# Optimization experiments

Measured on AMD Instinct MI355X. Metric: run time of the kernel, lower is better.

The kernel has to match this reference:

```python
import jax, jax.numpy as jnp
import numpy as np

N_NODES = 50000
N_EDGES = 500000
IN_CH = 128
OUT_CH = 64
HEADS = 4


def setup_inputs() -> dict:
    key = jax.random.key(0)
    ks = jax.random.split(key, 9)
    x = jax.random.normal(ks[0], (N_NODES, IN_CH), dtype=jnp.float32)
    edge_index = jax.random.randint(ks[1], (2, N_EDGES), 0, N_NODES, dtype=jnp.int64)
    edge_weights = jax.random.uniform(ks[2], (N_EDGES, 1), dtype=jnp.float32)
    # xavier-uniform params, stored as [in, out] so y = x @ W
    def xavier(k, shape):
        fan_in, fan_out = shape
        lim = float(np.sqrt(6.0 / (fan_in + fan_out)))
        return jax.random.uniform(k, shape, minval=-lim, maxval=lim, dtype=jnp.float32)
    Wq = xavier(ks[3], (IN_CH, OUT_CH * HEADS))
    Wk = xavier(ks[4], (IN_CH, OUT_CH * HEADS))
    Wv = xavier(ks[5], (IN_CH, OUT_CH * HEADS))
    We = xavier(ks[6], (1, HEADS))
    Wout = xavier(ks[7], (OUT_CH * HEADS, OUT_CH))
    b_out = jnp.zeros((OUT_CH,), dtype=jnp.float32)
    return {"x": x, "edge_index": edge_index, "edge_weights": edge_weights,
            "Wq": Wq, "Wk": Wk, "Wv": Wv, "We": We, "Wout": Wout, "b_out": b_out}


def reference(x, edge_index, edge_weights, Wq, Wk, Wv, We, Wout, b_out):
    num_nodes = x.shape[0]
    src = edge_index[0]
    tgt = edge_index[1]
    x_src = x[src]                                    # [E, in]
    x_tgt = x[tgt]                                    # [E, in]
    q = (x_tgt @ Wq).reshape(-1, HEADS, OUT_CH)       # [E, H, C]
    k = (x_src @ Wk).reshape(-1, HEADS, OUT_CH)
    v = (x_src @ Wv).reshape(-1, HEADS, OUT_CH)
    attn = jnp.sum(q * k, axis=-1) / jnp.sqrt(jnp.float32(OUT_CH))  # [E, H]
    attn = attn + edge_weights @ We                   # [E, H]
    attn = jax.nn.leaky_relu(attn, negative_slope=0.2)
    attn = jax.nn.softmax(attn, axis=0)               # global softmax over edges (as in source)
    weighted_v = attn[..., None] * v                  # [E, H, C]
    out = jax.ops.segment_sum(weighted_v, tgt, num_segments=num_nodes)  # [N, H, C]
    out = out.reshape(num_nodes, HEADS * OUT_CH) @ Wout + b_out         # [N, out]
    if x.shape == out.shape:
        out = out + x
    return out
```

## Files before the change

kernel.cpp:

```cpp
#include <hip/hip_runtime.h>
#include <hip/hip_bf16.h>
#include <hip/hip_fp16.h>

#define N_NODES 50000
#define N_EDGES 500000
#define IN_CH   128
#define D       256
#define UDIM    512
#define OUT_CH  64
#define HEADS   4
#define NC      49
#define PCAP    448
#define DEPTH   4

#define NB_X16  6250
#define NB_HIST 1954
#define NB_MB   256
#define NB_ZB   128
#define NB_GEMM 1564
#define NB_SCAT 1954
#define NB_K4   (NB_GEMM + NB_SCAT)
#define NB_OUT  782

typedef _Float16 half8 __attribute__((ext_vector_type(8)));
typedef _Float16 half2_t __attribute__((ext_vector_type(2)));
typedef float   floatx4 __attribute__((ext_vector_type(4)));

typedef __attribute__((address_space(1))) const void as1_void;
typedef __attribute__((address_space(3))) void as3_void;

__device__ __forceinline__ void gll16(const void* g, void* l) {
    __builtin_amdgcn_global_load_lds((as1_void*)g, (as3_void*)l, 16, 0, 0);
}

__device__ __forceinline__ float dpp_xor1(float x) {
    return __int_as_float(__builtin_amdgcn_mov_dpp(__float_as_int(x), 0xB1, 0xf, 0xf, true));
}
__device__ __forceinline__ float dpp_xor2(float x) {
    return __int_as_float(__builtin_amdgcn_mov_dpp(__float_as_int(x), 0x4E, 0xf, 0xf, true));
}

__global__ __launch_bounds__(256) void k1_prep_kernel(const float* __restrict__ x,
                                                      __half* __restrict__ x16,
                                                      const int* __restrict__ ei,
                                                      int* __restrict__ cnt,
                                                      double* __restrict__ S,
                                                      const float* __restrict__ Wq,
                                                      const float* __restrict__ Wk,
                                                      const float* __restrict__ Wv,
                                                      const float* __restrict__ Wout,
                                                      __half* __restrict__ M16t,
                                                      __half* __restrict__ Zc16t) {
    __shared__ float sbuf[4][64];
    const int b = blockIdx.x, tid = threadIdx.x;
    if (b < NB_X16) {
        int i = b * 256 + tid;
        if (i < HEADS) S[i] = 0.0;
        int k = i * 4;
        if (k < N_NODES * IN_CH) {
            float4 v = *(const float4*)(x + k);
            union { __half2 h[2]; uint2 u; } pk;
            pk.h[0] = __floats2half2_rn(v.x, v.y);
            pk.h[1] = __floats2half2_rn(v.z, v.w);
            *(uint2*)(x16 + k) = pk.u;
        }
    } else if (b < NB_X16 + NB_HIST) {
        int e = (b - NB_X16) * 256 + tid;
        if (e < N_EDGES) atomicAdd(&cnt[ei[N_EDGES + e]], 1);
    } else if (b < NB_X16 + NB_HIST + NB_MB) {
        const int r = (b - NB_X16 - NB_HIST) * 2 + (tid >> 7);
        const int i = tid & 127;
        const int h = r >> 7, j = r & 127;
        float* buf = sbuf[tid >> 7];
        if (i < 64) buf[i] = Wk[(size_t)j * D + h * 64 + i];
        __syncthreads();
        const float4* qr = (const float4*)(Wq + (size_t)i * D + h * 64);
        float s = 0.f;
        #pragma unroll
        for (int c4 = 0; c4 < 16; ++c4) {
            float4 q = qr[c4];
            s += q.x * buf[c4 * 4] + q.y * buf[c4 * 4 + 1]
               + q.z * buf[c4 * 4 + 2] + q.w * buf[c4 * 4 + 3];
        }
        M16t[(size_t)r * IN_CH + i] = __float2half(s);
    } else {
        const int r = (b - NB_X16 - NB_HIST - NB_MB) * 4 + (tid >> 6);
        const int c = tid & 63;
        const int h = r >> 7, i = r & 127;
        float* buf = sbuf[tid >> 6];
        buf[c] = Wv[(size_t)i * D + h * 64 + c];
        __syncthreads();
        float s = 0.f;
        #pragma unroll 8
        for (int j = 0; j < 64; ++j)
            s += buf[j] * Wout[(size_t)(h * 64 + j) * OUT_CH + c];
        Zc16t[(size_t)c * UDIM + r] = __float2half(s);
    }
}

__global__ __launch_bounds__(256) void k2_scan_reduce_kernel(const int* __restrict__ cnt,
                                                             int* __restrict__ csum) {
    const int b = blockIdx.x, tid = threadIdx.x;
    const int lane = tid & 63, wid = tid >> 6;
    int s = 0;
    int idx0 = b * 1024 + tid * 4;
    #pragma unroll
    for (int i = 0; i < 4; ++i) {
        int idx = idx0 + i;
        if (idx < N_NODES) s += cnt[idx];
    }
    #pragma unroll
    for (int m = 1; m < 64; m <<= 1) s += __shfl_xor(s, m, 64);
    __shared__ int w4[4];
    if (lane == 0) w4[wid] = s;
    __syncthreads();
    if (tid == 0) csum[b] = w4[0] + w4[1] + w4[2] + w4[3];
}

__global__ __launch_bounds__(256) void k3_scan_chunks_kernel(int* __restrict__ cnt,
                                                             const int* __restrict__ csum,
                                                             int* __restrict__ rp) {
    __shared__ int stop[64];
    __shared__ int wsum[4];
    const int b = blockIdx.x, tid = threadIdx.x;
    const int lane = tid & 63, wid = tid >> 6;
    if (tid < 64) stop[tid] = (tid < NC) ? csum[tid] : 0;
    __syncthreads();
    int base = 0;
    for (int w = 0; w < b; ++w) base += stop[w];
    int v[4];
    const int idx0 = b * 1024 + tid * 4;
    #pragma unroll
    for (int i = 0; i < 4; ++i) {
        int idx = idx0 + i;
        v[i] = (idx < N_NODES) ? cnt[idx] : 0;
    }
    int tsum = v[0] + v[1] + v[2] + v[3];
    int x = tsum;
    #pragma unroll
    for (int d = 1; d < 64; d <<= 1) {
        int y = __shfl_up(x, d, 64);
        if (lane >= d) x += y;
    }
    if (lane == 63) wsum[wid] = x;
    __syncthreads();
    int woff = 0;
    for (int w = 0; w < wid; ++w) woff += wsum[w];
    int excl = base + woff + x - tsum;
    #pragma unroll
    for (int i = 0; i < 4; ++i) {
        int idx = idx0 + i;
        if (idx < N_NODES) { rp[idx] = excl; cnt[idx] = excl; }
        excl += v[i];
    }
}

__global__ __launch_bounds__(256) void k4_gemmu_scatter_kernel(const __half* __restrict__ x16,
                                                               const __half* __restrict__ M16t,
                                                               __half* __restrict__ u16,
                                                               const int* __restrict__ ei,
                                                               const float* __restrict__ ew,
                                                               int* __restrict__ cnt,
                                                               int2* __restrict__ payload) {
    __shared__ __half Bm[128][136];
    const int tid = threadIdx.x;
    const int b = blockIdx.x;
    const int glo = (int)(((long long)b * NB_GEMM) / NB_K4);
    const int ghi = (int)(((long long)(b + 1) * NB_GEMM) / NB_K4);
    if (ghi == glo) {
        int e = (b - glo) * 256 + tid;
        if (e < N_EDGES) {
            int s = ei[e], t = ei[N_EDGES + e];
            int pos = atomicAdd(&cnt[t], 1);
            payload[pos] = make_int2(s, __float_as_int(ew[e]));
        }
        return;
    }
    const int m0 = (glo % 391) * 128;
    const int colbase = (glo / 391) * 128;
    {
        const int r = tid >> 1, part = tid & 1;
        const uint4* sb = (const uint4*)(M16t + (size_t)(colbase + r) * IN_CH + part * 64);
        uint4* db = (uint4*)&Bm[r][part * 64];
        #pragma unroll
        for (int q = 0; q < 8; ++q) db[q] = sb[q];
    }

    const int w = tid >> 6, lane = tid & 63;
    const int mrow = lane & 15, quad = lane >> 4;

    half8 a[2][4];
    #pragma unroll
    for (int mt = 0; mt < 2; ++mt) {
        int row = min(m0 + w * 32 + mt * 16 + mrow, N_NODES - 1);
        const __half* ab = x16 + (size_t)row * IN_CH + quad * 8;
        #pragma unroll
        for (int ks = 0; ks < 4; ++ks) a[mt][ks] = *(const half8*)(ab + ks * 32);
    }
    __syncthreads();

    floatx4 acc[2][8];
    #pragma unroll
    for (int mt = 0; mt < 2; ++mt)
        #pragma unroll
        for (int nt = 0; nt < 8; ++nt)
            acc[mt][nt] = (floatx4){0.f, 0.f, 0.f, 0.f};

    #pragma unroll
    for (int nt = 0; nt < 8; ++nt) {
        #pragma unroll
        for (int ks = 0; ks < 4; ++ks) {
            half8 bfr = *(const half8*)&Bm[nt * 16 + mrow][ks * 32 + quad * 8];
            acc[0][nt] = __builtin_amdgcn_mfma_f32_16x16x32_f16(a[0][ks], bfr, acc[0][nt], 0, 0, 0);
            acc[1][nt] = __builtin_amdgcn_mfma_f32_16x16x32_f16(a[1][ks], bfr, acc[1][nt], 0, 0, 0);
        }
    }
    __syncthreads();
    #pragma unroll
    for (int mt = 0; mt < 2; ++mt)
        #pragma unroll
        for (int nt = 0; nt < 8; ++nt)
            #pragma unroll
            for (int r = 0; r < 4; ++r)
                Bm[w * 32 + mt * 16 + quad * 4 + r][nt * 16 + mrow] = __float2half(acc[mt][nt][r]);
    __syncthreads();
    {
        const int r = tid >> 1, part = tid & 1;
        if (m0 + r < N_NODES) {
            const uint4* s4 = (const uint4*)&Bm[r][part * 64];
            uint4* d4 = (uint4*)(u16 + (size_t)(m0 + r) * UDIM + colbase + part * 64);
            #pragma unroll
            for (int q = 0; q < 8; ++q) d4[q] = s4[q];
        }
    }
}

__global__ __launch_bounds__(256) void edge_fused_kernel(const __half* __restrict__ u16,
                                                         const __half* __restrict__ x16,
                                                         const int* __restrict__ rp,
                                                         const int* __restrict__ cnt,
                                                         const int2* __restrict__ payload,
                                                         const float* __restrict__ We,
                                                         __half* __restrict__ y16,
                                                         double* __restrict__ S) {
    __shared__ __half xring[4][DEPTH][512];
    __shared__ int2 pbuf[PCAP];
    __shared__ float sblk[4];
    const int tid = threadIdx.x;
    const int nodebase = blockIdx.x * 16;

    const int span0 = rp[nodebase];
    const int span1 = cnt[nodebase + 15];
    const int span  = span1 - span0;
    const int span_len = min(span, PCAP);
    for (int i = tid; i < span_len; i += 256) pbuf[i] = payload[span0 + i];
    if (tid < 4) sblk[tid] = 0.f;
    __syncthreads();

    const int w = tid >> 6, lane = tid & 63;
    const int g = lane >> 4;
    const int l16 = lane & 15;
    const int h = l16 >> 2;
    const int q = l16 & 3;
    const int node = nodebase + (tid >> 4);
    const float wev = We[h];

    uint4 ur4[4];
    {
        const uint4* ub = (const uint4*)(u16 + (size_t)node * UDIM + h * 128 + q * 32);
        ur4[0] = ub[0]; ur4[1] = ub[1]; ur4[2] = ub[2]; ur4[3] = ub[3];
    }
    const half2_t* uh = (const half2_t*)ur4;

    half2_t yacc[16];
    #pragma unroll
    for (int t = 0; t < 16; ++t) yacc[t] = (half2_t){(_Float16)0.f, (_Float16)0.f};

    float sacc = 0.f;
    const int start = rp[node];
    const int end = cnt[node];
    const int ng = end - start;

    if (span <= PCAP) {
        int nmax = ng;
        nmax = max(nmax, __shfl_xor(nmax, 16, 64));
        nmax = max(nmax, __shfl_xor(nmax, 32, 64));
        if (nmax > 0) {
            const int chunk_off = (l16 ^ g) * 8;
            auto src_of = [&](int t) -> const __half* {
                int idx = min(start + t, end - 1);
                idx = max(idx, span0);
                int s = pbuf[idx - span0].x;
                return x16 + (size_t)s * IN_CH + chunk_off;
            };
            #pragma unroll
            for (int s = 0; s < DEPTH; ++s)
                gll16(src_of(s), &xring[w][s][0]);

            for (int t = 0; t < nmax; ++t) {
                const int slot = t & (DEPTH - 1);
                asm volatile("s_waitcnt vmcnt(3)" ::: "memory");
                __builtin_amdgcn_sched_barrier(0);
                const uint4* rb = (const uint4*)&xring[w][slot][g * 128 + q * 32];
                uint4 xr0 = rb[0 ^ g];
                uint4 xr1 = rb[1 ^ g];
                uint4 xr2 = rb[2 ^ g];
                uint4 xr3 = rb[3 ^ g];
                asm volatile("s_waitcnt lgkmcnt(0)" ::: "memory");
                __builtin_amdgcn_sched_barrier(0);
                gll16(src_of(t + DEPTH), &xring[w][slot][0]);

                int2 pl;
                {
                    int idx = min(start + t, end - 1);
                    idx = max(idx, span0);
                    pl = pbuf[idx - span0];
                }
                uint4 xr[4] = {xr0, xr1, xr2, xr3};
                const half2_t* xh = (const half2_t*)xr;
                float d0 = 0.f, d1 = 0.f, d2 = 0.f, d3 = 0.f;
                #pragma unroll
                for (int tt = 0; tt < 4; ++tt) {
                    d0 = __builtin_amdgcn_fdot2(uh[tt],      xh[tt],      d0, false);
                    d1 = __builtin_amdgcn_fdot2(uh[tt + 4],  xh[tt + 4],  d1, false);
                    d2 = __builtin_amdgcn_fdot2(uh[tt + 8],  xh[tt + 8],  d2, false);
                    d3 = __builtin_amdgcn_fdot2(uh[tt + 12], xh[tt + 12], d3, false);
                }
                float dot = (d0 + d1) + (d2 + d3);
                dot += dpp_xor1(dot);
                dot += dpp_xor2(dot);
                float l = dot * 0.125f + __int_as_float(pl.y) * wev;
                l = fmaxf(l, 0.2f * l);
                float p = __expf(l);
                if (t < ng) {
                    if (q == 0) sacc += p;
                    half2_t p2 = (half2_t){(_Float16)p, (_Float16)p};
                    #pragma unroll
                    for (int tt = 0; tt < 16; ++tt)
                        yacc[tt] = p2 * xh[tt] + yacc[tt];
                }
            }
        }
    } else {
        auto getpl = [&](int e) -> int2 {
            int idx = e - span0;
            return (idx < PCAP) ? pbuf[idx] : payload[e];
        };
        int2 pl = make_int2(0, 0);
        uint4 xr[4];
        if (start < end) {
            pl = getpl(start);
            const uint4* xb = (const uint4*)(x16 + (size_t)pl.x * IN_CH + q * 32);
            xr[0] = xb[0]; xr[1] = xb[1]; xr[2] = xb[2]; xr[3] = xb[3];
        }
        for (int e = start; e < end; ++e) {
            int2 pln = pl;
            uint4 xrn[4] = {xr[0], xr[1], xr[2], xr[3]};
            if (e + 1 < end) {
                pln = getpl(e + 1);
                const uint4* xb = (const uint4*)(x16 + (size_t)pln.x * IN_CH + q * 32);
                xrn[0] = xb[0]; xrn[1] = xb[1]; xrn[2] = xb[2]; xrn[3] = xb[3];
            }
            const half2_t* xh = (const half2_t*)xr;
            float dot = 0.f;
            #pragma unroll
            for (int t = 0; t < 16; ++t)
                dot = __builtin_amdgcn_fdot2(uh[t], xh[t], dot, false);
            dot += __shfl_xor(dot, 1, 16);
            dot += __shfl_xor(dot, 2, 16);
            float l = dot * 0.125f + __int_as_float(pl.y) * wev;
            l = fmaxf(l, 0.2f * l);
            float p = __expf(l);
            if (q == 0) sacc += p;
            half2_t p2 = (half2_t){(_Float16)p, (_Float16)p};
            #pragma unroll
            for (int t = 0; t < 16; ++t)
                yacc[t] = p2 * xh[t] + yacc[t];
            pl = pln;
            xr[0] = xrn[0]; xr[1] = xrn[1]; xr[2] = xrn[2]; xr[3] = xrn[3];
        }
    }
    {
        uint4* yo = (uint4*)(y16 + (size_t)node * UDIM + h * 128 + q * 32);
        const uint4* ys = (const uint4*)yacc;
        yo[0] = ys[0]; yo[1] = ys[1]; yo[2] = ys[2]; yo[3] = ys[3];
    }
    __syncthreads();
    if (q == 0) atomicAdd(&sblk[h], sacc);
    __syncthreads();
    if (tid < 4) atomicAdd(&S[tid], (double)sblk[tid]);
}

__global__ __launch_bounds__(256) void gemm_out_mfma_kernel(const __half* __restrict__ y16,
                                                            const __half* __restrict__ Zc16t,
                                                            const double* __restrict__ S,
                                                            const float* __restrict__ b_out,
                                                            float* __restrict__ out) {
    const int tid = threadIdx.x;
    const int w = tid >> 6, lane = tid & 63;
    const int mrow = lane & 15, quad = lane >> 4;
    const int row0 = blockIdx.x * 64 + w * 16;

    float invs[4];
    #pragma unroll
    for (int hh = 0; hh < HEADS; ++hh) invs[hh] = (float)(1.0 / S[hh]);

    floatx4 result[4];
    #pragma unroll
    for (int nt = 0; nt < 4; ++nt) result[nt] = (floatx4){0.f, 0.f, 0.f, 0.f};

    for (int h = 0; h < HEADS; ++h) {
        half8 a[4];
        {
            int arow = min(row0 + mrow, N_NODES - 1);
            const __half* ab = y16 + (size_t)arow * UDIM + h * 128 + quad * 8;
            #pragma unroll
            for (int ks = 0; ks < 4; ++ks) a[ks] = *(const half8*)(ab + ks * 32);
        }
        const float inv = invs[h];
        #pragma unroll
        for (int nt = 0; nt < 4; ++nt) {
            floatx4 acc = (floatx4){0.f, 0.f, 0.f, 0.f};
            const __half* bb = Zc16t + (size_t)(nt * 16 + mrow) * UDIM + h * 128 + quad * 8;
            #pragma unroll
            for (int ks = 0; ks < 4; ++ks) {
                half8 bfr = *(const half8*)(bb + ks * 32);
                acc = __builtin_amdgcn_mfma_f32_16x16x32_f16(a[ks], bfr, acc, 0, 0, 0);
            }
            result[nt][0] += inv * acc[0];
            result[nt][1] += inv * acc[1];
            result[nt][2] += inv * acc[2];
            result[nt][3] += inv * acc[3];
        }
    }
    float bcol[4];
    #pragma unroll
    for (int nt = 0; nt < 4; ++nt) bcol[nt] = b_out[nt * 16 + mrow];
    #pragma unroll
    for (int r = 0; r < 4; ++r) {
        int row = row0 + quad * 4 + r;
        if (row < N_NODES) {
            float* dst = out + (size_t)row * OUT_CH;
            #pragma unroll
            for (int nt = 0; nt < 4; ++nt)
                dst[nt * 16 + mrow] = result[nt][r] + bcol[nt];
        }
    }
}

extern "C" void kernel_launch(void* const* d_in, const int* in_sizes, int n_in,
                              void* d_out, int out_size, void* d_ws, size_t ws_size,
                              hipStream_t stream) {
    const float* x     = (const float*)d_in[0];
    const int*   ei    = (const int*)d_in[1];
    const float* ew    = (const float*)d_in[2];
    const float* Wq    = (const float*)d_in[3];
    const float* Wk    = (const float*)d_in[4];
    const float* Wv    = (const float*)d_in[5];
    const float* We    = (const float*)d_in[6];
    const float* Wout  = (const float*)d_in[7];
    const float* b_out = (const float*)d_in[8];
    float* out = (float*)d_out;

    __half* u16   = (__half*)d_ws;
    __half* y16   = u16 + (size_t)N_NODES * UDIM;
    __half* x16   = y16 + (size_t)N_NODES * UDIM;
    double* S     = (double*)(x16 + (size_t)N_NODES * IN_CH);
    __half* M16t  = (__half*)(S + HEADS);
    __half* Zc16t = M16t + UDIM * IN_CH;
    int*    rp    = (int*)(Zc16t + OUT_CH * UDIM);
    int*    cnt   = rp + N_NODES;
    int*    csum  = cnt + N_NODES;
    int2*   payload = (int2*)(csum + 64);

    hipMemsetAsync(cnt, 0, N_NODES * sizeof(int), stream);
    k1_prep_kernel<<<NB_X16 + NB_HIST + NB_MB + NB_ZB, 256, 0, stream>>>(
        x, x16, ei, cnt, S, Wq, Wk, Wv, Wout, M16t, Zc16t);
    k2_scan_reduce_kernel<<<NC, 256, 0, stream>>>(cnt, csum);
    k3_scan_chunks_kernel<<<NC, 256, 0, stream>>>(cnt, csum, rp);
    k4_gemmu_scatter_kernel<<<NB_K4, 256, 0, stream>>>(
        x16, M16t, u16, ei, ew, cnt, payload);
    edge_fused_kernel<<<N_NODES / 16, 256, 0, stream>>>(u16, x16, rp, cnt, payload, We, y16, S);
    gemm_out_mfma_kernel<<<NB_OUT, 256, 0, stream>>>(y16, Zc16t, S, b_out, out);
}
```

Measured before the change: 259.4 us.

## Fuse per-head output projection into edge kernel, add light finalize pass

The edge kernel now keeps its 16-node aggregated rows in LDS and runs the per-head MFMA projection against Zc16t in place, storing per-head partial outputs (N×256 fp16) instead of the full N×512 aggregate. A small finalize kernel then scales each head's partial by the global softmax denominator, sums the heads and adds the bias. This removes the write and re-read of the large y16 buffer and replaces the heavier output GEMM kernel with an elementwise pass. The cost is extra LDS and MFMA work inside the edge kernel, which may lower occupancy, plus fp16 rounding of the per-head partials before normalisation.

New measurement: 237.8 us. 8.3% less time.

```diff
diff --git a/kernel.cpp b/kernel.cpp
--- a/kernel.cpp
+++ b/kernel.cpp
@@ -20,7 +20,6 @@
 #define NB_GEMM 1564
 #define NB_SCAT 1954
 #define NB_K4   (NB_GEMM + NB_SCAT)
-#define NB_OUT  782
 
 typedef _Float16 half8 __attribute__((ext_vector_type(8)));
 typedef _Float16 half2_t __attribute__((ext_vector_type(2)));
@@ -241,9 +240,11 @@
                                                          const int* __restrict__ cnt,
                                                          const int2* __restrict__ payload,
                                                          const float* __restrict__ We,
-                                                         __half* __restrict__ y16,
+                                                         const __half* __restrict__ Zc16t,
+                                                         __half* __restrict__ p16,
                                                          double* __restrict__ S) {
     __shared__ __half xring[4][DEPTH][512];
+    __shared__ __half y_lds[16][520];
     __shared__ int2 pbuf[PCAP];
     __shared__ float sblk[4];
     const int tid = threadIdx.x;
@@ -381,71 +382,54 @@
         }
     }
     {
-        uint4* yo = (uint4*)(y16 + (size_t)node * UDIM + h * 128 + q * 32);
+        uint4* yo = (uint4*)&y_lds[tid >> 4][h * 128 + q * 32];
         const uint4* ys = (const uint4*)yacc;
         yo[0] = ys[0]; yo[1] = ys[1]; yo[2] = ys[2]; yo[3] = ys[3];
     }
-    __syncthreads();
     if (q == 0) atomicAdd(&sblk[h], sacc);
     __syncthreads();
     if (tid < 4) atomicAdd(&S[tid], (double)sblk[tid]);
-}
-
-__global__ __launch_bounds__(256) void gemm_out_mfma_kernel(const __half* __restrict__ y16,
-                                                            const __half* __restrict__ Zc16t,
-                                                            const double* __restrict__ S,
-                                                            const float* __restrict__ b_out,
-                                                            float* __restrict__ out) {
-    const int tid = threadIdx.x;
-    const int w = tid >> 6, lane = tid & 63;
-    const int mrow = lane & 15, quad = lane >> 4;
-    const int row0 = blockIdx.x * 64 + w * 16;
-
-    float invs[4];
-    #pragma unroll
-    for (int hh = 0; hh < HEADS; ++hh) invs[hh] = (float)(1.0 / S[hh]);
-
-    floatx4 result[4];
-    #pragma unroll
-    for (int nt = 0; nt < 4; ++nt) result[nt] = (floatx4){0.f, 0.f, 0.f, 0.f};
-
-    for (int h = 0; h < HEADS; ++h) {
-        half8 a[4];
-        {
-            int arow = min(row0 + mrow, N_NODES - 1);
-            const __half* ab = y16 + (size_t)arow * UDIM + h * 128 + quad * 8;
-            #pragma unroll
-            for (int ks = 0; ks < 4; ++ks) a[ks] = *(const half8*)(ab + ks * 32);
-        }
-        const float inv = invs[h];
+
+    {
+        const int hh = w;
+        const int mrow = lane & 15, quad = lane >> 4;
+        half8 a2[4];
+        #pragma unroll
+        for (int ks = 0; ks < 4; ++ks)
+            a2[ks] = *(const half8*)&y_lds[mrow][hh * 128 + ks * 32 + quad * 8];
         #pragma unroll
         for (int nt = 0; nt < 4; ++nt) {
             floatx4 acc = (floatx4){0.f, 0.f, 0.f, 0.f};
-            const __half* bb = Zc16t + (size_t)(nt * 16 + mrow) * UDIM + h * 128 + quad * 8;
+            const __half* bb = Zc16t + (size_t)(nt * 16 + mrow) * UDIM + hh * 128 + quad * 8;
             #pragma unroll
             for (int ks = 0; ks < 4; ++ks) {
                 half8 bfr = *(const half8*)(bb + ks * 32);
-                acc = __builtin_amdgcn_mfma_f32_16x16x32_f16(a[ks], bfr, acc, 0, 0, 0);
+                acc = __builtin_amdgcn_mfma_f32_16x16x32_f16(a2[ks], bfr, acc, 0, 0, 0);
             }
-            result[nt][0] += inv * acc[0];
-            result[nt][1] += inv * acc[1];
-            result[nt][2] += inv * acc[2];
-            result[nt][3] += inv * acc[3];
-        }
-    }
-    float bcol[4];
-    #pragma unroll
-    for (int nt = 0; nt < 4; ++nt) bcol[nt] = b_out[nt * 16 + mrow];
-    #pragma unroll
-    for (int r = 0; r < 4; ++r) {
-        int row = row0 + quad * 4 + r;
-        if (row < N_NODES) {
-            float* dst = out + (size_t)row * OUT_CH;
-            #pragma unroll
-            for (int nt = 0; nt < 4; ++nt)
-                dst[nt * 16 + mrow] = result[nt][r] + bcol[nt];
-        }
-    }
+            #pragma unroll
+            for (int r = 0; r < 4; ++r)
+                p16[(size_t)(nodebase + quad * 4 + r) * D + hh * 64 + nt * 16 + mrow] =
+                    __float2half(acc[r]);
+        }
+    }
+}
+
+__global__ __launch_bounds__(256) void finalize_kernel(const __half* __restrict__ p16,
+                                                       const double* __restrict__ S,
+                                                       const float* __restrict__ b_out,
+                                                       float* __restrict__ out) {
+    const int idx = blockIdx.x * 256 + threadIdx.x;
+    const int n = idx >> 6, c = idx & 63;
+    const float i0 = (float)(1.0 / S[0]);
+    const float i1 = (float)(1.0 / S[1]);
+    const float i2 = (float)(1.0 / S[2]);
+    const float i3 = (float)(1.0 / S[3]);
+    const __half* pr = p16 + (size_t)n * D + c;
+    float v = __half2float(pr[0])   * i0
+            + __half2float(pr[64])  * i1
+            + __half2float(pr[128]) * i2
+            + __half2float(pr[192]) * i3;
+    out[(size_t)n * OUT_CH + c] = v + b_out[c];
 }
 
 extern "C" void kernel_launch(void* const* d_in, const int* in_sizes, int n_in,
@@ -463,8 +447,8 @@
     float* out = (float*)d_out;
 
     __half* u16   = (__half*)d_ws;
-    __half* y16   = u16 + (size_t)N_NODES * UDIM;
-    __half* x16   = y16 + (size_t)N_NODES * UDIM;
+    __half* p16   = u16 + (size_t)N_NODES * UDIM;
+    __half* x16   = p16 + (size_t)N_NODES * UDIM;
     double* S     = (double*)(x16 + (size_t)N_NODES * IN_CH);
     __half* M16t  = (__half*)(S + HEADS);
     __half* Zc16t = M16t + UDIM * IN_CH;
@@ -480,6 +464,7 @@
     k3_scan_chunks_kernel<<<NC, 256, 0, stream>>>(cnt, csum, rp);
     k4_gemmu_scatter_kernel<<<NB_K4, 256, 0, stream>>>(
         x16, M16t, u16, ei, ew, cnt, payload);
-    edge_fused_kernel<<<N_NODES / 16, 256, 0, stream>>>(u16, x16, rp, cnt, payload, We, y16, S);
-    gemm_out_mfma_kernel<<<NB_OUT, 256, 0, stream>>>(y16, Zc16t, S, b_out, out);
-}
+    edge_fused_kernel<<<N_NODES / 16, 256, 0, stream>>>(
+        u16, x16, rp, cnt, payload, We, Zc16t, p16, S);
+    finalize_kernel<<<(N_NODES * OUT_CH) / 256, 256, 0, stream>>>(p16, S, b_out, out);
+}
```
